# Performance work log

Measured on AMD Instinct MI355X. Metric: run time of the kernel, lower is better.

Reference implementation:

```python
import jax, jax.numpy as jnp
import numpy as np

N_NODES = 100000
N_EDGES = 3200000
D_FEAT = 128


def setup_inputs() -> dict:
    key = jax.random.key(0)
    k1, k2, k3, k4 = jax.random.split(key, 4)
    rows = jax.random.randint(k1, (N_EDGES,), 0, N_NODES, dtype=jnp.int32)
    cols = jax.random.randint(k2, (N_EDGES,), 0, N_NODES, dtype=jnp.int32)
    vals = jax.random.uniform(k3, (N_EDGES,), dtype=jnp.float32)
    embeds = jax.random.normal(k4, (N_NODES, D_FEAT), dtype=jnp.float32)
    return {"rows": rows, "cols": cols, "vals": vals, "embeds": embeds}


def reference(rows, cols, vals, embeds):
    # out = adj @ embeds, adj in COO form: out[r] += vals[e] * embeds[cols[e]]
    gathered = vals[:, None] * embeds[cols]          # [E, D]
    out = jax.ops.segment_sum(gathered, rows, num_segments=N_NODES)  # [N, D]
    return out
```

## Files before the change

kernel.cpp:

```cpp
#include <hip/hip_runtime.h>

#define D_FEAT  128
#define RSHIFT  6
#define RPB     64
#define NB_MAX  2048
#define NBLK    512
#define BT      256
#define CAP     2432

#define CHSHIFT 13
#define NCH     16
#define SBINS   (RPB * NCH)

__global__ void zero_out_kernel(float* __restrict__ out, int n4) {
    int i = blockIdx.x * blockDim.x + threadIdx.x;
    if (i < n4) ((float4*)out)[i] = make_float4(0.f, 0.f, 0.f, 0.f);
}

__global__ void coo_scatter_atomic_kernel(const int* __restrict__ rows,
                                          const int* __restrict__ cols,
                                          const float* __restrict__ vals,
                                          const float* __restrict__ embeds,
                                          float* __restrict__ out,
                                          int n_edges) {
    int tid  = blockIdx.x * blockDim.x + threadIdx.x;
    int edge = tid >> 5;
    int lane = tid & 31;
    if (edge >= n_edges) return;
    int   r = rows[edge];
    int   c = cols[edge];
    float v = vals[edge];
    const float4* src = (const float4*)(embeds + (size_t)c * D_FEAT);
    float4 e = src[lane];
    float* dst = out + (size_t)r * D_FEAT + lane * 4;
    atomicAdd(dst + 0, v * e.x);
    atomicAdd(dst + 1, v * e.y);
    atomicAdd(dst + 2, v * e.z);
    atomicAdd(dst + 3, v * e.w);
}

__device__ inline unsigned short f2bf(float f) {
    unsigned int u = __float_as_uint(f);
    u += 0x7fffu + ((u >> 16) & 1u);
    return (unsigned short)(u >> 16);
}

__global__ __launch_bounds__(256) void conv_bf16_pack_kernel(const float* __restrict__ in,
                                                             uint2* __restrict__ out,
                                                             int n_nodes) {
    int tid = blockIdx.x * blockDim.x + threadIdx.x;
    int c = tid >> 5, l = tid & 31;
    if (c >= n_nodes) return;
    float4 f = ((const float4*)(in + (size_t)c * D_FEAT))[l];
    uint2 q;
    q.x = (unsigned)f2bf(f.x) | ((unsigned)f2bf(f.y) << 16);
    q.y = (unsigned)f2bf(f.z) | ((unsigned)f2bf(f.w) << 16);
    out[(size_t)c * 32 + l] = q;
}


__global__ __launch_bounds__(BT) void p1_count(const int* __restrict__ rows,
                                               int* __restrict__ Cmat,
                                               int n_edges, int nb, int tile) {
    __shared__ int cnt[NB_MAX];
    int blk = blockIdx.x, t = threadIdx.x;
    for (int b = t; b < nb; b += BT) cnt[b] = 0;
    __syncthreads();
    int e0 = blk * tile;
    int e1 = min(e0 + tile, n_edges);
    for (int i = e0 + t; i < e1; i += BT)
        atomicAdd(&cnt[rows[i] >> RSHIFT], 1);
    __syncthreads();
    int* dst = Cmat + (size_t)blk * nb;
    for (int b = t; b < nb; b += BT) dst[b] = cnt[b];
}

__global__ __launch_bounds__(NBLK) void s3_fused(const int* __restrict__ Cmat,
                                                 int* __restrict__ BmatT,
                                                 int* __restrict__ total, int nb) {
    __shared__ int s[NBLK];
    int b = blockIdx.x, t = threadIdx.x;
    int v = Cmat[(size_t)t * nb + b];
    s[t] = v;
    __syncthreads();
    for (int off = 1; off < NBLK; off <<= 1) {
        int u = (t >= off) ? s[t - off] : 0;
        __syncthreads();
        s[t] += u;
        __syncthreads();
    }
    BmatT[(size_t)b * NBLK + t] = s[t] - v;
    if (t == NBLK - 1) total[b] = s[t];
}

__global__ __launch_bounds__(1024) void s2_base(const int* __restrict__ total,
                                                int* __restrict__ base, int nb) {
    __shared__ int s[2048];
    int t = threadIdx.x;
    int v0 = (t < nb) ? total[t] : 0;
    int v1 = (t + 1024 < nb) ? total[t + 1024] : 0;
    s[t] = v0;
    s[t + 1024] = v1;
    __syncthreads();
    for (int off = 1; off < 2048; off <<= 1) {
        int u0 = (t >= off) ? s[t - off] : 0;
        int u1 = (t + 1024 >= off) ? s[t + 1024 - off] : 0;
        __syncthreads();
        s[t] += u0;
        s[t + 1024] += u1;
        __syncthreads();
    }
    if (t < nb)        base[t]        = s[t]        - v0;
    if (t + 1024 < nb) base[t + 1024] = s[t + 1024] - v1;
}

__global__ __launch_bounds__(BT) void p2_scatter(const int* __restrict__ rows,
                                                 const int* __restrict__ cols,
                                                 const float* __restrict__ vals,
                                                 const int* __restrict__ base,
                                                 const int* __restrict__ BmatT,
                                                 int2* __restrict__ pairs,
                                                 int n_edges, int nb, int tile) {
    __shared__ int curs[NB_MAX];
    int blk = blockIdx.x, t = threadIdx.x;
    for (int b = t; b < nb; b += BT)
        curs[b] = base[b] + BmatT[(size_t)b * NBLK + blk];
    __syncthreads();
    int e0 = blk * tile;
    int e1 = min(e0 + tile, n_edges);
    for (int i = e0 + t; i < e1; i += BT) {
        int   r = rows[i];
        int   c = cols[i];
        float v = vals[i];
        int   b = r >> RSHIFT;
        int pos = atomicAdd(&curs[b], 1);
        pairs[pos] = make_int2(c | ((r & (RPB - 1)) << 17), __float_as_int(v));
    }
}

__global__ __launch_bounds__(256) void sort_bucket_kernel(const int* __restrict__ total,
                                                          const int* __restrict__ base,
                                                          int2* __restrict__ pairs,
                                                          int* __restrict__ rowbeg,
                                                          int* __restrict__ rowend,
                                                          int n_rows) {
    __shared__ int2 stage[CAP];
    __shared__ int  hist[SBINS];
    __shared__ int  ex[SBINS + 1];
    __shared__ int  scan_s[256];

    int b = blockIdx.x, t = threadIdx.x;
    int n     = total[b];
    int pbase = base[b];
    if (n > CAP) n = CAP;

    for (int i = t; i < SBINS; i += 256) hist[i] = 0;
    __syncthreads();
    for (int i = t; i < n; i += 256) {
        int x = pairs[pbase + i].x;
        int key = (((x >> 17) & (RPB - 1)) << 4) | ((x >> CHSHIFT) & (NCH - 1));
        atomicAdd(&hist[key], 1);
    }
    __syncthreads();
    int h0 = hist[4 * t], h1 = hist[4 * t + 1], h2 = hist[4 * t + 2], h3 = hist[4 * t + 3];
    int local = h0 + h1 + h2 + h3;
    scan_s[t] = local;
    __syncthreads();
    for (int off = 1; off < 256; off <<= 1) {
        int u = (t >= off) ? scan_s[t - off] : 0;
        __syncthreads();
        scan_s[t] += u;
        __syncthreads();
    }
    int bt = scan_s[t] - local;
    ex[4 * t]     = bt;
    ex[4 * t + 1] = bt + h0;
    ex[4 * t + 2] = bt + h0 + h1;
    ex[4 * t + 3] = bt + h0 + h1 + h2;
    hist[4 * t]     = bt;
    hist[4 * t + 1] = bt + h0;
    hist[4 * t + 2] = bt + h0 + h1;
    hist[4 * t + 3] = bt + h0 + h1 + h2;
    if (t == 255) ex[SBINS] = bt + local;
    __syncthreads();

    for (int i = t; i < n; i += 256) {
        int2 p  = pairs[pbase + i];
        int key = (((p.x >> 17) & (RPB - 1)) << 4) | ((p.x >> CHSHIFT) & (NCH - 1));
        int pos = atomicAdd(&hist[key], 1);
        stage[pos] = make_int2(p.x & 0x1FFFF, p.y);
    }
    __syncthreads();

    for (int i = t; i < n; i += 256) pairs[pbase + i] = stage[i];
    if (t < RPB) {
        int row = (b << RSHIFT) + t;
        if (row < n_rows) {
            rowbeg[row] = pbase + ex[t << 4];
            rowend[row] = pbase + ex[(t + 1) << 4];
        }
    }
}

template <bool BF16>
__global__ __launch_bounds__(256, 4) void reduce_row_kernel(const int* __restrict__ rowbeg,
                                                            const int* __restrict__ rowend,
                                                            const int2* __restrict__ pairs,
                                                            const float* __restrict__ embF,
                                                            const uint2* __restrict__ embB,
                                                            float* __restrict__ out,
                                                            int n_rows) {
    int g    = threadIdx.x >> 5;
    int lane = threadIdx.x & 31;
    int row  = (blockIdx.x << 3) + g;
    if (row >= n_rows) return;
    int s0 = rowbeg[row];
    int s1 = rowend[row];
    float4 acc = make_float4(0.f, 0.f, 0.f, 0.f);

#define GATH(p, q) (BF16 ? (void)((q) = embB[(size_t)((p).x) * 32 + lane]) : (void)0)

    int i = s0;
    for (; i + 7 < s1; i += 8) {
        int2 p0 = pairs[i + 0], p1 = pairs[i + 1], p2 = pairs[i + 2], p3 = pairs[i + 3];
        int2 p4 = pairs[i + 4], p5 = pairs[i + 5], p6 = pairs[i + 6], p7 = pairs[i + 7];
        if (BF16) {
            uint2 q0 = embB[(size_t)p0.x * 32 + lane];
            uint2 q1 = embB[(size_t)p1.x * 32 + lane];
            uint2 q2 = embB[(size_t)p2.x * 32 + lane];
            uint2 q3 = embB[(size_t)p3.x * 32 + lane];
            uint2 q4 = embB[(size_t)p4.x * 32 + lane];
            uint2 q5 = embB[(size_t)p5.x * 32 + lane];
            uint2 q6 = embB[(size_t)p6.x * 32 + lane];
            uint2 q7 = embB[(size_t)p7.x * 32 + lane];
#define ACC(pp, qq) {                                                        \
            float v = __int_as_float((pp).y);                                \
            acc.x += v * __uint_as_float((qq).x << 16);                      \
            acc.y += v * __uint_as_float((qq).x & 0xffff0000u);              \
            acc.z += v * __uint_as_float((qq).y << 16);                      \
            acc.w += v * __uint_as_float((qq).y & 0xffff0000u); }
            ACC(p0, q0); ACC(p1, q1); ACC(p2, q2); ACC(p3, q3);
            ACC(p4, q4); ACC(p5, q5); ACC(p6, q6); ACC(p7, q7);
#undef ACC
        } else {
            const float4* e4 = (const float4*)embF;
            float4 q0 = e4[(size_t)p0.x * 32 + lane];
            float4 q1 = e4[(size_t)p1.x * 32 + lane];
            float4 q2 = e4[(size_t)p2.x * 32 + lane];
            float4 q3 = e4[(size_t)p3.x * 32 + lane];
            float4 q4 = e4[(size_t)p4.x * 32 + lane];
            float4 q5 = e4[(size_t)p5.x * 32 + lane];
            float4 q6 = e4[(size_t)p6.x * 32 + lane];
            float4 q7 = e4[(size_t)p7.x * 32 + lane];
#define ACCF(pp, qq) {                                                       \
            float v = __int_as_float((pp).y);                                \
            acc.x += v * (qq).x; acc.y += v * (qq).y;                        \
            acc.z += v * (qq).z; acc.w += v * (qq).w; }
            ACCF(p0, q0); ACCF(p1, q1); ACCF(p2, q2); ACCF(p3, q3);
            ACCF(p4, q4); ACCF(p5, q5); ACCF(p6, q6); ACCF(p7, q7);
#undef ACCF
        }
    }
    for (; i < s1; ++i) {
        int2 p = pairs[i];
        float v = __int_as_float(p.y);
        if (BF16) {
            uint2 q = embB[(size_t)p.x * 32 + lane];
            acc.x += v * __uint_as_float(q.x << 16);
            acc.y += v * __uint_as_float(q.x & 0xffff0000u);
            acc.z += v * __uint_as_float(q.y << 16);
            acc.w += v * __uint_as_float(q.y & 0xffff0000u);
        } else {
            float4 q = ((const float4*)embF)[(size_t)p.x * 32 + lane];
            acc.x += v * q.x; acc.y += v * q.y; acc.z += v * q.z; acc.w += v * q.w;
        }
    }
#undef GATH
    ((float4*)(out + (size_t)row * D_FEAT))[lane] = acc;
}

extern "C" void kernel_launch(void* const* d_in, const int* in_sizes, int n_in,
                              void* d_out, int out_size, void* d_ws, size_t ws_size,
                              hipStream_t stream) {
    const int*   rows   = (const int*)d_in[0];
    const int*   cols   = (const int*)d_in[1];
    const float* vals   = (const float*)d_in[2];
    const float* embeds = (const float*)d_in[3];
    float*       out    = (float*)d_out;

    const int n_edges = in_sizes[0];
    const int n_rows  = out_size / D_FEAT;
    const int n_nodes = in_sizes[3] / D_FEAT;

    const int nb = (n_rows + RPB - 1) >> RSHIFT;

    size_t cmat_b  = (((size_t)NBLK * nb * sizeof(int)) + 255) & ~(size_t)255;
    size_t bmatT_b = (((size_t)nb * NBLK * sizeof(int)) + 255) & ~(size_t)255;
    size_t tot_b   = (((size_t)nb * sizeof(int)) + 255) & ~(size_t)255;
    size_t base_b  = tot_b;
    size_t pair_b  = (((size_t)n_edges * sizeof(int2)) + 255) & ~(size_t)255;
    size_t rbeg_b  = (((size_t)n_rows * sizeof(int)) + 255) & ~(size_t)255;
    size_t rend_b  = rbeg_b;
    size_t embB_b  = (size_t)n_nodes * D_FEAT * sizeof(unsigned short);
    size_t need0   = cmat_b + bmatT_b + tot_b + base_b + pair_b + rbeg_b + rend_b;
    size_t need1   = need0 + embB_b;

    bool ok = (ws_size >= need0) && (nb <= NB_MAX) &&
              (n_nodes <= (1 << 17)) && (n_rows <= (1 << 17));
    if (!ok) {
        int out_n4 = out_size / 4;
        zero_out_kernel<<<(out_n4 + 255) / 256, 256, 0, stream>>>(out, out_n4);
        long long totalT = (long long)n_edges * 32;
        int grid = (int)((totalT + 255) / 256);
        coo_scatter_atomic_kernel<<<grid, 256, 0, stream>>>(rows, cols, vals, embeds, out, n_edges);
        return;
    }
    bool use_bf16 = (ws_size >= need1);

    char* ws = (char*)d_ws;
    int*   Cmat   = (int*)ws;    ws += cmat_b;
    int*   BmatT  = (int*)ws;    ws += bmatT_b;
    int*   total  = (int*)ws;    ws += tot_b;
    int*   base   = (int*)ws;    ws += base_b;
    int2*  pairs  = (int2*)ws;   ws += pair_b;
    int*   rowbeg = (int*)ws;    ws += rbeg_b;
    int*   rowend = (int*)ws;    ws += rend_b;
    uint2* embB   = (uint2*)ws;

    int tile = (n_edges + NBLK - 1) / NBLK;

    if (use_bf16) {
        int nthreads = n_nodes * 32;
        conv_bf16_pack_kernel<<<(nthreads + 255) / 256, 256, 0, stream>>>(embeds, embB, n_nodes);
    }
    p1_count  <<<NBLK, BT,   0, stream>>>(rows, Cmat, n_edges, nb, tile);
    s3_fused  <<<nb,   NBLK, 0, stream>>>(Cmat, BmatT, total, nb);
    s2_base   <<<1,    1024, 0, stream>>>(total, base, nb);
    p2_scatter<<<NBLK, BT,   0, stream>>>(rows, cols, vals, base, BmatT, pairs,
                                          n_edges, nb, tile);
    sort_bucket_kernel<<<nb, 256, 0, stream>>>(total, base, pairs, rowbeg, rowend, n_rows);

    int rgrid = (n_rows + 7) / 8;
    if (use_bf16)
        reduce_row_kernel<true><<<rgrid, 256, 0, stream>>>(rowbeg, rowend, pairs,
                                                           embeds, embB, out, n_rows);
    else
        reduce_row_kernel<false><<<rgrid, 256, 0, stream>>>(rowbeg, rowend, pairs,
                                                            embeds, embB, out, n_rows);
}
```

Before: 351.4 us.

## Stage bucket scatter in LDS for contiguous global writes

The partition scatter kernel now does a local counting sort of each block's edge tile in shared memory, using a block-wide prefix scan over its per-bucket counts. It then writes the staged pairs out linearly, so consecutive threads write mostly contiguous runs within each bucket instead of random 8-byte scattered stores. The block count drops to 256 with 512 threads each so that a tile fits the roughly 125 KB LDS stage buffer. The trade-offs are very high LDS use (one block per CU), an extra scan and sync, and fewer, larger tiles in the count and scatter passes.

```diff
diff --git a/kernel.cpp b/kernel.cpp
--- a/kernel.cpp
+++ b/kernel.cpp
@@ -4,7 +4,9 @@
 #define RSHIFT  6
 #define RPB     64
 #define NB_MAX  2048
-#define NBLK    512
+#define NBLK    256
+#define P2T     512
+#define P2CAP   12544
 #define BT      256
 #define CAP     2432
 
@@ -59,20 +61,20 @@
 }
 
 
-__global__ __launch_bounds__(BT) void p1_count(const int* __restrict__ rows,
-                                               int* __restrict__ Cmat,
-                                               int n_edges, int nb, int tile) {
+__global__ __launch_bounds__(P2T) void p1_count(const int* __restrict__ rows,
+                                                int* __restrict__ Cmat,
+                                                int n_edges, int nb, int tile) {
     __shared__ int cnt[NB_MAX];
     int blk = blockIdx.x, t = threadIdx.x;
-    for (int b = t; b < nb; b += BT) cnt[b] = 0;
+    for (int b = t; b < nb; b += P2T) cnt[b] = 0;
     __syncthreads();
     int e0 = blk * tile;
     int e1 = min(e0 + tile, n_edges);
-    for (int i = e0 + t; i < e1; i += BT)
+    for (int i = e0 + t; i < e1; i += P2T)
         atomicAdd(&cnt[rows[i] >> RSHIFT], 1);
     __syncthreads();
     int* dst = Cmat + (size_t)blk * nb;
-    for (int b = t; b < nb; b += BT) dst[b] = cnt[b];
+    for (int b = t; b < nb; b += P2T) dst[b] = cnt[b];
 }
 
 __global__ __launch_bounds__(NBLK) void s3_fused(const int* __restrict__ Cmat,
@@ -114,27 +116,64 @@
     if (t + 1024 < nb) base[t + 1024] = s[t + 1024] - v1;
 }
 
-__global__ __launch_bounds__(BT) void p2_scatter(const int* __restrict__ rows,
-                                                 const int* __restrict__ cols,
-                                                 const float* __restrict__ vals,
-                                                 const int* __restrict__ base,
-                                                 const int* __restrict__ BmatT,
-                                                 int2* __restrict__ pairs,
-                                                 int n_edges, int nb, int tile) {
-    __shared__ int curs[NB_MAX];
+__global__ __launch_bounds__(P2T) void p2_scatter(const int* __restrict__ rows,
+                                                  const int* __restrict__ cols,
+                                                  const float* __restrict__ vals,
+                                                  const int* __restrict__ base,
+                                                  const int* __restrict__ BmatT,
+                                                  const int* __restrict__ Cmat,
+                                                  int2* __restrict__ pairs,
+                                                  int n_edges, int nb, int tile) {
+    __shared__ int2           stage[P2CAP];
+    __shared__ unsigned short bkt[P2CAP];
+    __shared__ int            lcur[NB_MAX];
+    __shared__ int            goff[NB_MAX];
+    __shared__ int            scan_s[P2T];
+
     int blk = blockIdx.x, t = threadIdx.x;
-    for (int b = t; b < nb; b += BT)
-        curs[b] = base[b] + BmatT[(size_t)b * NBLK + blk];
-    __syncthreads();
+
+    const int* crow = Cmat + (size_t)blk * nb;
+    int b0 = t << 2;
+    int c0 = (b0     < nb) ? crow[b0]     : 0;
+    int c1 = (b0 + 1 < nb) ? crow[b0 + 1] : 0;
+    int c2 = (b0 + 2 < nb) ? crow[b0 + 2] : 0;
+    int c3 = (b0 + 3 < nb) ? crow[b0 + 3] : 0;
+    int local = c0 + c1 + c2 + c3;
+    scan_s[t] = local;
+    __syncthreads();
+    for (int off = 1; off < P2T; off <<= 1) {
+        int u = (t >= off) ? scan_s[t - off] : 0;
+        __syncthreads();
+        scan_s[t] += u;
+        __syncthreads();
+    }
+    int e = scan_s[t] - local;
+    if (b0     < nb) { lcur[b0]     = e; goff[b0]     = base[b0]     + BmatT[(size_t)(b0)     * NBLK + blk] - e; }
+    e += c0;
+    if (b0 + 1 < nb) { lcur[b0 + 1] = e; goff[b0 + 1] = base[b0 + 1] + BmatT[(size_t)(b0 + 1) * NBLK + blk] - e; }
+    e += c1;
+    if (b0 + 2 < nb) { lcur[b0 + 2] = e; goff[b0 + 2] = base[b0 + 2] + BmatT[(size_t)(b0 + 2) * NBLK + blk] - e; }
+    e += c2;
+    if (b0 + 3 < nb) { lcur[b0 + 3] = e; goff[b0 + 3] = base[b0 + 3] + BmatT[(size_t)(b0 + 3) * NBLK + blk] - e; }
+    __syncthreads();
+
     int e0 = blk * tile;
     int e1 = min(e0 + tile, n_edges);
-    for (int i = e0 + t; i < e1; i += BT) {
+    int ntile = e1 - e0;
+    for (int i = e0 + t; i < e1; i += P2T) {
         int   r = rows[i];
         int   c = cols[i];
         float v = vals[i];
         int   b = r >> RSHIFT;
-        int pos = atomicAdd(&curs[b], 1);
-        pairs[pos] = make_int2(c | ((r & (RPB - 1)) << 17), __float_as_int(v));
+        int pos = atomicAdd(&lcur[b], 1);
+        stage[pos] = make_int2(c | ((r & (RPB - 1)) << 17), __float_as_int(v));
+        bkt[pos]   = (unsigned short)b;
+    }
+    __syncthreads();
+
+    for (int i = t; i < ntile; i += P2T) {
+        int b = bkt[i];
+        pairs[goff[b] + i] = stage[i];
     }
 }
 
@@ -217,8 +256,6 @@
     int s0 = rowbeg[row];
     int s1 = rowend[row];
     float4 acc = make_float4(0.f, 0.f, 0.f, 0.f);
-
-#define GATH(p, q) (BF16 ? (void)((q) = embB[(size_t)((p).x) * 32 + lane]) : (void)0)
 
     int i = s0;
     for (; i + 7 < s1; i += 8) {
@@ -275,7 +312,6 @@
             acc.x += v * q.x; acc.y += v * q.y; acc.z += v * q.z; acc.w += v * q.w;
         }
     }
-#undef GATH
     ((float4*)(out + (size_t)row * D_FEAT))[lane] = acc;
 }
 
@@ -292,7 +328,8 @@
     const int n_rows  = out_size / D_FEAT;
     const int n_nodes = in_sizes[3] / D_FEAT;
 
-    const int nb = (n_rows + RPB - 1) >> RSHIFT;
+    const int nb   = (n_rows + RPB - 1) >> RSHIFT;
+    const int tile = (n_edges + NBLK - 1) / NBLK;
 
     size_t cmat_b  = (((size_t)NBLK * nb * sizeof(int)) + 255) & ~(size_t)255;
     size_t bmatT_b = (((size_t)nb * NBLK * sizeof(int)) + 255) & ~(size_t)255;
@@ -305,7 +342,7 @@
     size_t need0   = cmat_b + bmatT_b + tot_b + base_b + pair_b + rbeg_b + rend_b;
     size_t need1   = need0 + embB_b;
 
-    bool ok = (ws_size >= need0) && (nb <= NB_MAX) &&
+    bool ok = (ws_size >= need0) && (nb <= NB_MAX) && (tile <= P2CAP) &&
               (n_nodes <= (1 << 17)) && (n_rows <= (1 << 17));
     if (!ok) {
         int out_n4 = out_size / 4;
@@ -327,16 +364,14 @@
     int*   rowend = (int*)ws;    ws += rend_b;
     uint2* embB   = (uint2*)ws;
 
-    int tile = (n_edges + NBLK - 1) / NBLK;
-
     if (use_bf16) {
         int nthreads = n_nodes * 32;
         conv_bf16_pack_kernel<<<(nthreads + 255) / 256, 256, 0, stream>>>(embeds, embB, n_nodes);
     }
-    p1_count  <<<NBLK, BT,   0, stream>>>(rows, Cmat, n_edges, nb, tile);
+    p1_count  <<<NBLK, P2T,  0, stream>>>(rows, Cmat, n_edges, nb, tile);
     s3_fused  <<<nb,   NBLK, 0, stream>>>(Cmat, BmatT, total, nb);
     s2_base   <<<1,    1024, 0, stream>>>(total, base, nb);
-    p2_scatter<<<NBLK, BT,   0, stream>>>(rows, cols, vals, base, BmatT, pairs,
+    p2_scatter<<<NBLK, P2T,  0, stream>>>(rows, cols, vals, base, BmatT, Cmat, pairs,
                                           n_edges, nb, tile);
     sort_bucket_kernel<<<nb, 256, 0, stream>>>(total, base, pairs, rowbeg, rowend, n_rows);
 
```

Result: faster. 302.0 us (-14.1%).
